# Kernel optimization log

Measured on AMD Instinct MI355X. Metric: run time of the kernel, lower is better.

Reference implementation:

```python
import jax, jax.numpy as jnp
import numpy as np

B, M, SV, OV, R, L, V, E = 256, 10, 32, 32, 128, 12, 1000, 64
M2 = M * M
STATE_DIM = (SV + 1) * M2  # 3300
OBJ_DIM = OV * M2          # 3200


def setup_inputs() -> dict:
    key = jax.random.key(0)
    ks = jax.random.split(key, 24)
    s = 0.02
    inp = {
        "state": jax.random.randint(ks[0], (B, M2), 0, SV),
        "obj": jax.random.randint(ks[1], (B, M2), 0, OV),
        "text": jax.random.randint(ks[2], (B, L), 0, V),
        # state MLP [STATE_DIM,128,128,R]
        "Ws1": jax.random.normal(ks[3], (STATE_DIM, 128)) * s,
        "bs1": jnp.zeros((128,)),
        "Ws2": jax.random.normal(ks[4], (128, 128)) * s,
        "bs2": jnp.zeros((128,)),
        "Ws3": jax.random.normal(ks[5], (128, R)) * s,
        "bs3": jnp.zeros((R,)),
        # object MLP [OBJ_DIM,128,128,R]
        "Wo1": jax.random.normal(ks[6], (OBJ_DIM, 128)) * s,
        "bo1": jnp.zeros((128,)),
        "Wo2": jax.random.normal(ks[7], (128, 128)) * s,
        "bo2": jnp.zeros((128,)),
        "Wo3": jax.random.normal(ks[8], (128, R)) * s,
        "bo3": jnp.zeros((R,)),
        # LSTM text encoder: embedding + single-layer LSTM with hidden=R
        "emb": jax.random.normal(ks[9], (V, E)) * s,
        "Wih": jax.random.normal(ks[10], (E, 4 * R)) * s,
        "Whh": jax.random.normal(ks[11], (R, 4 * R)) * s,
        "b_lstm": jnp.zeros((4 * R,)),
    }
    return inp


def _mlp(x, W1, b1, W2, b2, W3, b3):
    h = jax.nn.relu(x @ W1 + b1)
    h = jax.nn.relu(h @ W2 + b2)
    return h @ W3 + b3


def _lstm_last_hidden(text, emb, Wih, Whh, b):
    # text: (B, L) ids -> final hidden (B, R)
    x = emb[text]                      # (B, L, E)
    xs = jnp.swapaxes(x, 0, 1)         # (L, B, E)
    h0 = jnp.zeros((text.shape[0], R), x.dtype)
    c0 = jnp.zeros((text.shape[0], R), x.dtype)

    def step(carry, xt):
        h, c = carry
        g = xt @ Wih + h @ Whh + b     # (B, 4R)
        i, f, gg, o = jnp.split(g, 4, axis=-1)
        c = jax.nn.sigmoid(f) * c + jax.nn.sigmoid(i) * jnp.tanh(gg)
        h = jax.nn.sigmoid(o) * jnp.tanh(c)
        return (h, c), None

    (h, _), _ = jax.lax.scan(step, (h0, c0), xs)
    return h


def reference(state, obj, text, Ws1, bs1, Ws2, bs2, Ws3, bs3,
              Wo1, bo1, Wo2, bo2, Wo3, bo3, emb, Wih, Whh, b_lstm):
    b = state.shape[0]
    # one-hot encodings (torch scatter_ over channel dim)
    state_oh = jax.nn.one_hot(state, SV, dtype=jnp.float32)   # (B, 100, SV)
    obj_oh = jax.nn.one_hot(obj, OV, dtype=jnp.float32)       # (B, 100, OV)

    # repeat each map map_dim^2 times; copy p gets a one-hot of agent position p
    pos = jnp.eye(M2, dtype=jnp.float32)[None, :, :, None]    # (1, 100 copies, 100 cells, 1)
    state_rep = jnp.broadcast_to(state_oh[:, None], (b, M2, M2, SV))
    state_inp = jnp.concatenate(
        [state_rep, jnp.broadcast_to(pos, (b, M2, M2, 1))], axis=-1
    ).reshape(b * M2, STATE_DIM)
    obj_inp = jnp.broadcast_to(obj_oh[:, None], (b, M2, M2, OV)).reshape(b * M2, OBJ_DIM)

    state_out = _mlp(state_inp, Ws1, bs1, Ws2, bs2, Ws3, bs3)   # (B*100, R)
    object_out = _mlp(obj_inp, Wo1, bo1, Wo2, bo2, Wo3, bo3)    # (B*100, R)

    # text is identical across the 100 copies -> encode once, broadcast
    h = _lstm_last_hidden(text, emb, Wih, Whh, b_lstm)          # (B, R)
    lstm_out = jnp.broadcast_to(h[:, None], (b, M2, R)).reshape(b * M2, R)

    values = state_out * object_out * lstm_out                 # (B*100, R)
    map_pred = values.sum(1).reshape(b, M, M)
    return map_pred
```

## Files before the change

### kernel.cpp

```cpp
#include <hip/hip_runtime.h>


#define B_   256
#define M2_  100
#define R_   128
#define L_   12
#define E_   64

typedef _Float16 half2v __attribute__((ext_vector_type(2)));
typedef _Float16 f16x8  __attribute__((ext_vector_type(8)));
typedef float    f32x4  __attribute__((ext_vector_type(4)));

__device__ __forceinline__ float sigf(float x) { return 1.f / (1.f + expf(-x)); }

__device__ __forceinline__ uint pk16(float a, float b) {
    half2v h; h.x = (_Float16)a; h.y = (_Float16)b;
    return __builtin_bit_cast(uint, h);
}

#define PINU4(v) asm volatile("" : "+v"(v.x), "+v"(v.y), "+v"(v.z), "+v"(v.w));

__global__ __launch_bounds__(256) void pack_kernel(
    const float* __restrict__ Whh, const float* __restrict__ Wih,
    const float* __restrict__ Ws2, void* __restrict__ wsv)
{
    _Float16* WhhT = (_Float16*)wsv;
    _Float16* WihT = WhhT + 65536;
    uint*     W2P  = (uint*)(WihT + 32768);
    int g = blockIdx.x * 256 + threadIdx.x;
    if (g < 65536) {
        int r = g >> 9, c = g & 511;
        WhhT[c * 128 + r] = (_Float16)Whh[r * 512 + c];
    } else if (g < 65536 + 32768) {
        int g2 = g - 65536;
        int e = g2 >> 9, c = g2 & 511;
        WihT[c * 64 + e] = (_Float16)Wih[e * 512 + c];
    } else if (g < 65536 + 32768 + 8192) {
        int g3 = g - 65536 - 32768;
        int jp = g3 >> 7, kk = g3 & 127;
        W2P[g3] = pk16(Ws2[(2 * jp) * R_ + kk], Ws2[(2 * jp + 1) * R_ + kk]);
    }
}

__global__ __launch_bounds__(1024) __attribute__((amdgpu_waves_per_eu(4, 4)))
void k1_kernel(
    const int* __restrict__ state, const int* __restrict__ obj, const int* __restrict__ text,
    const float* __restrict__ Ws1, const float* __restrict__ bs1,
    const float* __restrict__ Wo1, const float* __restrict__ bo1,
    const float* __restrict__ Wo2, const float* __restrict__ bo2,
    const float* __restrict__ Wo3, const float* __restrict__ bo3,
    const float* __restrict__ emb, const float* __restrict__ b_lstm,
    const _Float16* __restrict__ WhhT, const _Float16* __restrict__ WihT,
    float* __restrict__ wsH, float* __restrict__ wsO3, float* __restrict__ wsBS)
{
    const int tid = threadIdx.x;
    __shared__ __align__(16) uint  U[9248];
    __shared__ __align__(16) float part[1024];
    __shared__ __align__(16) float hbuf[R_];
    __shared__ __align__(16) uint  hpair[R_ / 2];
    __shared__ __align__(16) float tmp[R_], tmp2[R_];
    __shared__ int idx[M2_], tids[L_];

    const int k = tid & 127, qq = tid >> 7;

    if (blockIdx.x < 256) {
        const int b    = blockIdx.x;
        const int lane = tid & 63;
        const int wv   = tid >> 6;
        const int m16  = lane & 15;
        const int kgrp = lane >> 4;
        float* xw   = (float*)U;
        float* xemb = (float*)(U + 8192);

        uint4 afu[2][4];
        #pragma unroll
        for (int tt = 0; tt < 2; ++tt) {
            int col = (2 * wv + tt) * 16 + m16;
            #pragma unroll
            for (int s = 0; s < 4; ++s) {
                afu[tt][s] = *(const uint4*)&WhhT[col * 128 + s * 32 + kgrp * 8];
                PINU4(afu[tt][s])
            }
        }

        if (tid < L_) tids[tid] = text[b * L_ + tid];
        if (tid >= 64 && tid < 128) hpair[tid - 64] = 0u;
        __syncthreads();
        if (tid < L_ * E_) xemb[(tid >> 6) * 66 + (tid & 63)] = emb[tids[tid >> 6] * E_ + (tid & 63)];
        else ((float*)(U + 8192 + 792))[tid - L_ * E_] = 0.f;
        __syncthreads();

        {
            f16x8 ax[2];
            #pragma unroll
            for (int s = 0; s < 2; ++s) {
                #pragma unroll
                for (int e = 0; e < 8; ++e)
                    ax[s][e] = (_Float16)xemb[m16 * 66 + s * 32 + kgrp * 8 + e];
            }
            #pragma unroll
            for (int h = 0; h < 2; ++h) {
                int col = (wv * 2 + h) * 16 + m16;
                float bl = b_lstm[col];
                f32x4 acc = { bl, bl, bl, bl };
                #pragma unroll
                for (int s = 0; s < 2; ++s) {
                    f16x8 bx = *(const f16x8*)&WihT[col * 64 + s * 32 + kgrp * 8];
                    acc = __builtin_amdgcn_mfma_f32_16x16x32_f16(ax[s], bx, acc, 0, 0, 0);
                }
                if (kgrp < 3) {
                    #pragma unroll
                    for (int r = 0; r < 4; ++r)
                        xw[(kgrp * 4 + r) * 512 + col] = acc[r];
                }
            }
        }
        __syncthreads();

        float cst = 0.f;
        for (int t = 0; t < L_; ++t) {
            f16x8 bf[4];
            #pragma unroll
            for (int s = 0; s < 4; ++s) {
                uint4 hb = *(const uint4*)&hpair[s * 16 + kgrp * 4];
                bf[s] = __builtin_bit_cast(f16x8, hb);
            }
            #pragma unroll
            for (int tt = 0; tt < 2; ++tt) {
                int colb = (2 * wv + tt) * 16 + kgrp * 4;
                f32x4 acc = *(const f32x4*)&xw[t * 512 + colb];
                #pragma unroll
                for (int s = 0; s < 4; ++s)
                    acc = __builtin_amdgcn_mfma_f32_16x16x32_f16(
                        __builtin_bit_cast(f16x8, afu[tt][s]), bf[s], acc, 0, 0, 0);
                if (m16 == 0) {
                    part[colb + 0] = acc[0];
                    part[colb + 1] = acc[1];
                    part[colb + 2] = acc[2];
                    part[colb + 3] = acc[3];
                }
            }
            __syncthreads();
            if (tid < R_) {
                float gi = part[tid], gf = part[R_ + tid], gg = part[2 * R_ + tid], go = part[3 * R_ + tid];
                cst = sigf(gf) * cst + sigf(gi) * tanhf(gg);
                float hn = sigf(go) * tanhf(cst);
                hbuf[tid] = hn;
                float hs = __shfl_down(hn, 1, 64);
                if (!(tid & 1)) hpair[tid >> 1] = pk16(hn, hs);
            }
            __syncthreads();
        }
        if (tid < R_) wsH[b * R_ + tid] = hbuf[tid];

    } else if (blockIdx.x < 512) {
        const int b = blockIdx.x - 256;
        if (tid < M2_) idx[tid] = obj[b * M2_ + tid];
        __syncthreads();
        {
            float acc = 0.f;
            int c0i = qq * 13, c1i = c0i + 13 < M2_ ? c0i + 13 : M2_;
            for (int c = c0i; c < c1i; ++c)
                acc += Wo1[(c * 32 + idx[c]) * R_ + k];
            part[qq * R_ + k] = acc;
        }
        __syncthreads();
        if (tid < R_) {
            float a = bo1[tid];
            #pragma unroll
            for (int q8 = 0; q8 < 8; ++q8) a += part[q8 * R_ + tid];
            tmp[tid] = fmaxf(a, 0.f);
        }
        __syncthreads();
        {
            float s0 = 0.f, s1 = 0.f, s2 = 0.f, s3 = 0.f;
            int j0 = qq * 16;
            #pragma unroll
            for (int j = 0; j < 16; j += 4) {
                s0 = fmaf(tmp[j0 + j + 0], Wo2[(j0 + j + 0) * R_ + k], s0);
                s1 = fmaf(tmp[j0 + j + 1], Wo2[(j0 + j + 1) * R_ + k], s1);
                s2 = fmaf(tmp[j0 + j + 2], Wo2[(j0 + j + 2) * R_ + k], s2);
                s3 = fmaf(tmp[j0 + j + 3], Wo2[(j0 + j + 3) * R_ + k], s3);
            }
            part[qq * R_ + k] = (s0 + s1) + (s2 + s3);
        }
        __syncthreads();
        if (tid < R_) {
            float a = bo2[tid];
            #pragma unroll
            for (int q8 = 0; q8 < 8; ++q8) a += part[q8 * R_ + tid];
            tmp2[tid] = fmaxf(a, 0.f);
        }
        __syncthreads();
        {
            float s0 = 0.f, s1 = 0.f, s2 = 0.f, s3 = 0.f;
            int j0 = qq * 16;
            #pragma unroll
            for (int j = 0; j < 16; j += 4) {
                s0 = fmaf(tmp2[j0 + j + 0], Wo3[(j0 + j + 0) * R_ + k], s0);
                s1 = fmaf(tmp2[j0 + j + 1], Wo3[(j0 + j + 1) * R_ + k], s1);
                s2 = fmaf(tmp2[j0 + j + 2], Wo3[(j0 + j + 2) * R_ + k], s2);
                s3 = fmaf(tmp2[j0 + j + 3], Wo3[(j0 + j + 3) * R_ + k], s3);
            }
            part[qq * R_ + k] = (s0 + s1) + (s2 + s3);
        }
        __syncthreads();
        if (tid < R_) {
            float a = bo3[tid];
            #pragma unroll
            for (int q8 = 0; q8 < 8; ++q8) a += part[q8 * R_ + tid];
            wsO3[b * R_ + tid] = a;
        }

    } else {
        const int b = blockIdx.x - 512;
        if (tid < M2_) idx[tid] = state[b * M2_ + tid];
        __syncthreads();
        {
            float acc = 0.f;
            int c0i = qq * 13, c1i = c0i + 13 < M2_ ? c0i + 13 : M2_;
            for (int c = c0i; c < c1i; ++c)
                acc += Ws1[(c * 33 + idx[c]) * R_ + k];
            part[qq * R_ + k] = acc;
        }
        __syncthreads();
        if (tid < R_) {
            float a = bs1[tid];
            #pragma unroll
            for (int q8 = 0; q8 < 8; ++q8) a += part[q8 * R_ + tid];
            wsBS[b * R_ + tid] = a;
        }
    }
}

__global__ __launch_bounds__(1024) __attribute__((amdgpu_waves_per_eu(4, 4)))
void k2_kernel(
    const float* __restrict__ Ws1, const float* __restrict__ bs2,
    const float* __restrict__ Ws3, const float* __restrict__ bs3,
    const uint* __restrict__ W2P,
    const float* __restrict__ wsH, const float* __restrict__ wsO3,
    const float* __restrict__ wsBS,
    float* __restrict__ out)
{
    const int b   = blockIdx.x;
    const int tid = threadIdx.x;

    __shared__ __align__(16) uint  U[16064];
    __shared__ __align__(16) float part[1024];
    __shared__ __align__(16) float wbuf[R_], ubuf[R_], bsbuf[R_];
    __shared__ float redw2[2][112];
    __shared__ float c0s;

    const int lane = tid & 63;
    const int wv   = tid >> 6;
    const int m16  = lane & 15;
    const int kgrp = lane >> 4;
    const int k = tid & 127, qq = tid >> 7;

    if (tid < R_) {
        wbuf[tid]  = wsH[b * R_ + tid] * wsO3[b * R_ + tid];
        bsbuf[tid] = wsBS[b * R_ + tid];
    }
    {
        const uint4* src = (const uint4*)W2P;
        #pragma unroll
        for (int idx = tid; idx < 2048; idx += 1024) {
            uint4 v = src[idx];
            int jp = idx >> 5, kq = idx & 31;
            *(uint4*)&U[jp * 132 + kq * 4] = v;
        }
    }
    __syncthreads();

    {
        float s0 = 0.f, s1 = 0.f, s2 = 0.f, s3 = 0.f;
        int j0 = qq * 16;
        const float4* w3 = reinterpret_cast<const float4*>(&Ws3[k * R_ + j0]);
        #pragma unroll
        for (int jj = 0; jj < 4; ++jj) {
            float4 v = w3[jj];
            s0 = fmaf(v.x, wbuf[j0 + jj * 4 + 0], s0);
            s1 = fmaf(v.y, wbuf[j0 + jj * 4 + 1], s1);
            s2 = fmaf(v.z, wbuf[j0 + jj * 4 + 2], s2);
            s3 = fmaf(v.w, wbuf[j0 + jj * 4 + 3], s3);
        }
        part[qq * R_ + k] = (s0 + s1) + (s2 + s3);
    }
    if (tid >= 960) {
        int j = tid - 960;
        float s = bs3[j] * wbuf[j] + bs3[j + 64] * wbuf[j + 64];
        s += __shfl_down(s, 32, 64);
        s += __shfl_down(s, 16, 64);
        s += __shfl_down(s, 8, 64);
        s += __shfl_down(s, 4, 64);
        s += __shfl_down(s, 2, 64);
        s += __shfl_down(s, 1, 64);
        if (j == 0) c0s = s;
    }
    #pragma unroll 4
    for (int pass = 0; pass < 13; ++pass) {
        int idx = pass * 1024 + tid;
        if (idx < M2_ * R_) {
            int j = idx & 127, p = idx >> 7;
            float v = fmaxf(bsbuf[j] + Ws1[(p * 33 + 32) * R_ + j], 0.f);
            float v2 = __shfl_down(v, 1, 64);
            if (!(j & 1)) U[8448 + p * 68 + (j >> 1)] = pk16(v, v2);
        }
    }
    if (tid < 816) U[8448 + 6800 + tid] = 0u;
    __syncthreads();
    if (tid < R_) {
        float a = 0.f;
        #pragma unroll
        for (int q8 = 0; q8 < 8; ++q8) a += part[q8 * R_ + tid];
        ubuf[tid] = a;
    }
    __syncthreads();

    if (wv < 14) {
        const int mtile = wv >> 1, nhalf = wv & 1;
        const uint* Ap = U + 8448 + (mtile * 16 + m16) * 68;
        f16x8 A[4];
        #pragma unroll
        for (int s = 0; s < 4; ++s)
            A[s] = __builtin_bit_cast(f16x8, *(const uint4*)&Ap[s * 16 + kgrp * 4]);
        f32x4 acc[4] = { {0,0,0,0}, {0,0,0,0}, {0,0,0,0}, {0,0,0,0} };
        #pragma unroll
        for (int nt = 0; nt < 4; ++nt) {
            int ko = (nhalf * 4 + nt) * 16 + m16;
            #pragma unroll
            for (int s = 0; s < 4; ++s) {
                const uint* Bp = U + (s * 16 + kgrp * 4) * 132 + ko;
                uint4 bv = { Bp[0], Bp[132], Bp[264], Bp[396] };
                acc[nt] = __builtin_amdgcn_mfma_f32_16x16x32_f16(
                    A[s], __builtin_bit_cast(f16x8, bv), acc[nt], 0, 0, 0);
            }
        }
        float vs0 = 0.f, vs1 = 0.f, vs2 = 0.f, vs3 = 0.f;
        #pragma unroll
        for (int nt = 0; nt < 4; ++nt) {
            int ko = (nhalf * 4 + nt) * 16 + m16;
            float bb = bs2[ko], uu = ubuf[ko];
            vs0 = fmaf(fmaxf(acc[nt][0] + bb, 0.f), uu, vs0);
            vs1 = fmaf(fmaxf(acc[nt][1] + bb, 0.f), uu, vs1);
            vs2 = fmaf(fmaxf(acc[nt][2] + bb, 0.f), uu, vs2);
            vs3 = fmaf(fmaxf(acc[nt][3] + bb, 0.f), uu, vs3);
        }
        vs0 += __shfl_xor(vs0, 1, 64); vs0 += __shfl_xor(vs0, 2, 64);
        vs0 += __shfl_xor(vs0, 4, 64); vs0 += __shfl_xor(vs0, 8, 64);
        vs1 += __shfl_xor(vs1, 1, 64); vs1 += __shfl_xor(vs1, 2, 64);
        vs1 += __shfl_xor(vs1, 4, 64); vs1 += __shfl_xor(vs1, 8, 64);
        vs2 += __shfl_xor(vs2, 1, 64); vs2 += __shfl_xor(vs2, 2, 64);
        vs2 += __shfl_xor(vs2, 4, 64); vs2 += __shfl_xor(vs2, 8, 64);
        vs3 += __shfl_xor(vs3, 1, 64); vs3 += __shfl_xor(vs3, 2, 64);
        vs3 += __shfl_xor(vs3, 4, 64); vs3 += __shfl_xor(vs3, 8, 64);
        if (m16 == 0) {
            int pr = mtile * 16 + kgrp * 4;
            redw2[nhalf][pr + 0] = vs0;
            redw2[nhalf][pr + 1] = vs1;
            redw2[nhalf][pr + 2] = vs2;
            redw2[nhalf][pr + 3] = vs3;
        }
    }
    __syncthreads();

    if (tid < M2_)
        out[b * M2_ + tid] = c0s + redw2[0][tid] + redw2[1][tid];
}

extern "C" void kernel_launch(void* const* d_in, const int* in_sizes, int n_in,
                              void* d_out, int out_size, void* d_ws, size_t ws_size,
                              hipStream_t stream) {
    const int*   state  = (const int*)d_in[0];
    const int*   obj    = (const int*)d_in[1];
    const int*   text   = (const int*)d_in[2];
    const float* Ws1    = (const float*)d_in[3];
    const float* bs1    = (const float*)d_in[4];
    const float* Ws2    = (const float*)d_in[5];
    const float* bs2    = (const float*)d_in[6];
    const float* Ws3    = (const float*)d_in[7];
    const float* bs3    = (const float*)d_in[8];
    const float* Wo1    = (const float*)d_in[9];
    const float* bo1    = (const float*)d_in[10];
    const float* Wo2    = (const float*)d_in[11];
    const float* bo2    = (const float*)d_in[12];
    const float* Wo3    = (const float*)d_in[13];
    const float* bo3    = (const float*)d_in[14];
    const float* emb    = (const float*)d_in[15];
    const float* Wih    = (const float*)d_in[16];
    const float* Whh    = (const float*)d_in[17];
    const float* b_lstm = (const float*)d_in[18];
    float* out = (float*)d_out;

    _Float16* WhhT = (_Float16*)d_ws;
    _Float16* WihT = WhhT + 65536;
    uint*     W2P  = (uint*)(WihT + 32768);
    float*    wsH  = (float*)(W2P + 8192);
    float*    wsO3 = wsH + 32768;
    float*    wsBS = wsO3 + 32768;

    hipLaunchKernelGGL(pack_kernel, dim3(416), dim3(256), 0, stream, Whh, Wih, Ws2, d_ws);
    hipLaunchKernelGGL(k1_kernel, dim3(768), dim3(1024), 0, stream,
                       state, obj, text, Ws1, bs1,
                       Wo1, bo1, Wo2, bo2, Wo3, bo3, emb, b_lstm,
                       WhhT, WihT, wsH, wsO3, wsBS);
    hipLaunchKernelGGL(k2_kernel, dim3(B_), dim3(1024), 0, stream,
                       Ws1, bs2, Ws3, bs3, W2P, wsH, wsO3, wsBS, out);
}
```

Baseline: 42.38 us.

## Halve block sizes, fuse LSTM gates in-register, move H1 build into k1

```diff
diff --git a/kernel.cpp b/kernel.cpp
--- a/kernel.cpp
+++ b/kernel.cpp
@@ -42,7 +42,7 @@
     }
 }
 
-__global__ __launch_bounds__(1024) __attribute__((amdgpu_waves_per_eu(4, 4)))
+__global__ __launch_bounds__(512) __attribute__((amdgpu_waves_per_eu(4, 4)))
 void k1_kernel(
     const int* __restrict__ state, const int* __restrict__ obj, const int* __restrict__ text,
     const float* __restrict__ Ws1, const float* __restrict__ bs1,
@@ -51,17 +51,14 @@
     const float* __restrict__ Wo3, const float* __restrict__ bo3,
     const float* __restrict__ emb, const float* __restrict__ b_lstm,
     const _Float16* __restrict__ WhhT, const _Float16* __restrict__ WihT,
-    float* __restrict__ wsH, float* __restrict__ wsO3, float* __restrict__ wsBS)
+    float* __restrict__ wsH, float* __restrict__ wsO3, uint* __restrict__ wsH1)
 {
     const int tid = threadIdx.x;
-    __shared__ __align__(16) uint  U[9248];
-    __shared__ __align__(16) float part[1024];
-    __shared__ __align__(16) float hbuf[R_];
-    __shared__ __align__(16) uint  hpair[R_ / 2];
-    __shared__ __align__(16) float tmp[R_], tmp2[R_];
+    __shared__ __align__(16) uint  U[7232];
+    __shared__ __align__(16) uint  hpair[2][64];
+    __shared__ __align__(16) float part[512];
+    __shared__ __align__(16) float tmp[R_], tmp2[R_], bsb[R_];
     __shared__ int idx[M2_], tids[L_];
-
-    const int k = tid & 127, qq = tid >> 7;
 
     if (blockIdx.x < 256) {
         const int b    = blockIdx.x;
@@ -70,37 +67,38 @@
         const int m16  = lane & 15;
         const int kgrp = lane >> 4;
         float* xw   = (float*)U;
-        float* xemb = (float*)(U + 8192);
-
-        uint4 afu[2][4];
-        #pragma unroll
-        for (int tt = 0; tt < 2; ++tt) {
-            int col = (2 * wv + tt) * 16 + m16;
+        float* xemb = (float*)(U + 6144);
+
+        uint4 afu[4][4];
+        #pragma unroll
+        for (int g = 0; g < 4; ++g) {
+            int col = (wv + 8 * g) * 16 + m16;
             #pragma unroll
             for (int s = 0; s < 4; ++s) {
-                afu[tt][s] = *(const uint4*)&WhhT[col * 128 + s * 32 + kgrp * 8];
-                PINU4(afu[tt][s])
+                afu[g][s] = *(const uint4*)&WhhT[col * 128 + s * 32 + kgrp * 8];
+                PINU4(afu[g][s])
             }
         }
 
         if (tid < L_) tids[tid] = text[b * L_ + tid];
-        if (tid >= 64 && tid < 128) hpair[tid - 64] = 0u;
-        __syncthreads();
-        if (tid < L_ * E_) xemb[(tid >> 6) * 66 + (tid & 63)] = emb[tids[tid >> 6] * E_ + (tid & 63)];
-        else ((float*)(U + 8192 + 792))[tid - L_ * E_] = 0.f;
+        if (tid >= 64 && tid < 128) hpair[0][tid - 64] = 0u;
+        __syncthreads();
+        for (int i = tid; i < 16 * 68; i += 512) {
+            int t = i / 68, c = i - t * 68;
+            xemb[i] = (c < 64 && t < L_) ? emb[tids[t] * E_ + c] : 0.f;
+        }
         __syncthreads();
 
         {
             f16x8 ax[2];
             #pragma unroll
-            for (int s = 0; s < 2; ++s) {
+            for (int s = 0; s < 2; ++s)
                 #pragma unroll
                 for (int e = 0; e < 8; ++e)
-                    ax[s][e] = (_Float16)xemb[m16 * 66 + s * 32 + kgrp * 8 + e];
-            }
-            #pragma unroll
-            for (int h = 0; h < 2; ++h) {
-                int col = (wv * 2 + h) * 16 + m16;
+                    ax[s][e] = (_Float16)xemb[m16 * 68 + s * 32 + kgrp * 8 + e];
+            #pragma unroll
+            for (int i4 = 0; i4 < 4; ++i4) {
+                int col = (wv + 8 * i4) * 16 + m16;
                 float bl = b_lstm[col];
                 f32x4 acc = { bl, bl, bl, bl };
                 #pragma unroll
@@ -117,66 +115,67 @@
         }
         __syncthreads();
 
-        float cst = 0.f;
+        float cst0 = 0.f, cst1 = 0.f, cst2 = 0.f, cst3 = 0.f;
+        float h0 = 0.f, h1v = 0.f, h2v = 0.f, h3v = 0.f;
         for (int t = 0; t < L_; ++t) {
+            const uint* hp = hpair[t & 1];
             f16x8 bf[4];
             #pragma unroll
-            for (int s = 0; s < 4; ++s) {
-                uint4 hb = *(const uint4*)&hpair[s * 16 + kgrp * 4];
-                bf[s] = __builtin_bit_cast(f16x8, hb);
-            }
-            #pragma unroll
-            for (int tt = 0; tt < 2; ++tt) {
-                int colb = (2 * wv + tt) * 16 + kgrp * 4;
-                f32x4 acc = *(const f32x4*)&xw[t * 512 + colb];
+            for (int s = 0; s < 4; ++s)
+                bf[s] = __builtin_bit_cast(f16x8, *(const uint4*)&hp[s * 16 + kgrp * 4]);
+            f32x4 acc[4];
+            #pragma unroll
+            for (int g = 0; g < 4; ++g) {
+                acc[g] = *(const f32x4*)&xw[t * 512 + (wv + 8 * g) * 16 + kgrp * 4];
                 #pragma unroll
                 for (int s = 0; s < 4; ++s)
-                    acc = __builtin_amdgcn_mfma_f32_16x16x32_f16(
-                        __builtin_bit_cast(f16x8, afu[tt][s]), bf[s], acc, 0, 0, 0);
-                if (m16 == 0) {
-                    part[colb + 0] = acc[0];
-                    part[colb + 1] = acc[1];
-                    part[colb + 2] = acc[2];
-                    part[colb + 3] = acc[3];
-                }
+                    acc[g] = __builtin_amdgcn_mfma_f32_16x16x32_f16(
+                        __builtin_bit_cast(f16x8, afu[g][s]), bf[s], acc[g], 0, 0, 0);
+            }
+            cst0 = sigf(acc[1][0]) * cst0 + sigf(acc[0][0]) * tanhf(acc[2][0]);
+            h0   = sigf(acc[3][0]) * tanhf(cst0);
+            cst1 = sigf(acc[1][1]) * cst1 + sigf(acc[0][1]) * tanhf(acc[2][1]);
+            h1v  = sigf(acc[3][1]) * tanhf(cst1);
+            cst2 = sigf(acc[1][2]) * cst2 + sigf(acc[0][2]) * tanhf(acc[2][2]);
+            h2v  = sigf(acc[3][2]) * tanhf(cst2);
+            cst3 = sigf(acc[1][3]) * cst3 + sigf(acc[0][3]) * tanhf(acc[2][3]);
+            h3v  = sigf(acc[3][3]) * tanhf(cst3);
+            if (m16 == 0) {
+                uint* hw = hpair[(t + 1) & 1];
+                hw[8 * wv + kgrp * 2]     = pk16(h0, h1v);
+                hw[8 * wv + kgrp * 2 + 1] = pk16(h2v, h3v);
             }
             __syncthreads();
-            if (tid < R_) {
-                float gi = part[tid], gf = part[R_ + tid], gg = part[2 * R_ + tid], go = part[3 * R_ + tid];
-                cst = sigf(gf) * cst + sigf(gi) * tanhf(gg);
-                float hn = sigf(go) * tanhf(cst);
-                hbuf[tid] = hn;
-                float hs = __shfl_down(hn, 1, 64);
-                if (!(tid & 1)) hpair[tid >> 1] = pk16(hn, hs);
-            }
-            __syncthreads();
-        }
-        if (tid < R_) wsH[b * R_ + tid] = hbuf[tid];
-
-    } else if (blockIdx.x < 512) {
+        }
+        if (m16 == 0) {
+            int j = wv * 16 + kgrp * 4;
+            wsH[b * R_ + j + 0] = h0;
+            wsH[b * R_ + j + 1] = h1v;
+            wsH[b * R_ + j + 2] = h2v;
+            wsH[b * R_ + j + 3] = h3v;
+        }
+
+    } else {
         const int b = blockIdx.x - 256;
+        const int k = tid & 127, qq = tid >> 7;
         if (tid < M2_) idx[tid] = obj[b * M2_ + tid];
         __syncthreads();
         {
-            float acc = 0.f;
-            int c0i = qq * 13, c1i = c0i + 13 < M2_ ? c0i + 13 : M2_;
-            for (int c = c0i; c < c1i; ++c)
-                acc += Wo1[(c * 32 + idx[c]) * R_ + k];
-            part[qq * R_ + k] = acc;
-        }
-        __syncthreads();
-        if (tid < R_) {
-            float a = bo1[tid];
-            #pragma unroll
-            for (int q8 = 0; q8 < 8; ++q8) a += part[q8 * R_ + tid];
-            tmp[tid] = fmaxf(a, 0.f);
-        }
+            float a = 0.f;
+            #pragma unroll 5
+            for (int c = qq * 25; c < qq * 25 + 25; ++c)
+                a += Wo1[(c * 32 + idx[c]) * R_ + k];
+            part[qq * R_ + k] = a;
+        }
+        __syncthreads();
+        if (tid < R_)
+            tmp[tid] = fmaxf(bo1[tid] + part[tid] + part[R_ + tid] + part[2 * R_ + tid] + part[3 * R_ + tid], 0.f);
         __syncthreads();
         {
             float s0 = 0.f, s1 = 0.f, s2 = 0.f, s3 = 0.f;
-            int j0 = qq * 16;
-            #pragma unroll
-            for (int j = 0; j < 16; j += 4) {
+            int j0 = qq * 32;
+            #pragma unroll
+            for (int j = 0; j < 32; j += 4) {
                 s0 = fmaf(tmp[j0 + j + 0], Wo2[(j0 + j + 0) * R_ + k], s0);
                 s1 = fmaf(tmp[j0 + j + 1], Wo2[(j0 + j + 1) * R_ + k], s1);
                 s2 = fmaf(tmp[j0 + j + 2], Wo2[(j0 + j + 2) * R_ + k], s2);
@@ -185,18 +184,14 @@
             part[qq * R_ + k] = (s0 + s1) + (s2 + s3);
         }
         __syncthreads();
-        if (tid < R_) {
-            float a = bo2[tid];
-            #pragma unroll
-            for (int q8 = 0; q8 < 8; ++q8) a += part[q8 * R_ + tid];
-            tmp2[tid] = fmaxf(a, 0.f);
-        }
+        if (tid < R_)
+            tmp2[tid] = fmaxf(bo2[tid] + part[tid] + part[R_ + tid] + part[2 * R_ + tid] + part[3 * R_ + tid], 0.f);
         __syncthreads();
         {
             float s0 = 0.f, s1 = 0.f, s2 = 0.f, s3 = 0.f;
-            int j0 = qq * 16;
-            #pragma unroll
-            for (int j = 0; j < 16; j += 4) {
+            int j0 = qq * 32;
+            #pragma unroll
+            for (int j = 0; j < 32; j += 4) {
                 s0 = fmaf(tmp2[j0 + j + 0], Wo3[(j0 + j + 0) * R_ + k], s0);
                 s1 = fmaf(tmp2[j0 + j + 1], Wo3[(j0 + j + 1) * R_ + k], s1);
                 s2 = fmaf(tmp2[j0 + j + 2], Wo3[(j0 + j + 2) * R_ + k], s2);
@@ -205,50 +200,48 @@
             part[qq * R_ + k] = (s0 + s1) + (s2 + s3);
         }
         __syncthreads();
-        if (tid < R_) {
-            float a = bo3[tid];
-            #pragma unroll
-            for (int q8 = 0; q8 < 8; ++q8) a += part[q8 * R_ + tid];
-            wsO3[b * R_ + tid] = a;
-        }
-
-    } else {
-        const int b = blockIdx.x - 512;
+        if (tid < R_)
+            wsO3[b * R_ + tid] = bo3[tid] + part[tid] + part[R_ + tid] + part[2 * R_ + tid] + part[3 * R_ + tid];
+        __syncthreads();
         if (tid < M2_) idx[tid] = state[b * M2_ + tid];
         __syncthreads();
         {
-            float acc = 0.f;
-            int c0i = qq * 13, c1i = c0i + 13 < M2_ ? c0i + 13 : M2_;
-            for (int c = c0i; c < c1i; ++c)
-                acc += Ws1[(c * 33 + idx[c]) * R_ + k];
-            part[qq * R_ + k] = acc;
-        }
-        __syncthreads();
-        if (tid < R_) {
-            float a = bs1[tid];
-            #pragma unroll
-            for (int q8 = 0; q8 < 8; ++q8) a += part[q8 * R_ + tid];
-            wsBS[b * R_ + tid] = a;
-        }
-    }
-}
-
-__global__ __launch_bounds__(1024) __attribute__((amdgpu_waves_per_eu(4, 4)))
+            float a = 0.f;
+            #pragma unroll 5
+            for (int c = qq * 25; c < qq * 25 + 25; ++c)
+                a += Ws1[(c * 33 + idx[c]) * R_ + k];
+            part[qq * R_ + k] = a;
+        }
+        __syncthreads();
+        if (tid < R_)
+            bsb[tid] = bs1[tid] + part[tid] + part[R_ + tid] + part[2 * R_ + tid] + part[3 * R_ + tid];
+        __syncthreads();
+        #pragma unroll 5
+        for (int pass = 0; pass < 25; ++pass) {
+            int id2 = pass * 512 + tid;
+            int j = id2 & 127, p = id2 >> 7;
+            float v = fmaxf(bsb[j] + Ws1[(p * 33 + 32) * R_ + j], 0.f);
+            float v2 = __shfl_down(v, 1, 64);
+            if (!(j & 1)) wsH1[(size_t)b * 7616 + p * 68 + (j >> 1)] = pk16(v, v2);
+        }
+    }
+}
+
+__global__ __launch_bounds__(512)
 void k2_kernel(
-    const float* __restrict__ Ws1, const float* __restrict__ bs2,
-    const float* __restrict__ Ws3, const float* __restrict__ bs3,
-    const uint* __restrict__ W2P,
+    const float* __restrict__ bs2, const float* __restrict__ Ws3,
+    const float* __restrict__ bs3, const uint* __restrict__ W2P,
     const float* __restrict__ wsH, const float* __restrict__ wsO3,
-    const float* __restrict__ wsBS,
+    const uint* __restrict__ wsH1,
     float* __restrict__ out)
 {
     const int b   = blockIdx.x;
     const int tid = threadIdx.x;
 
     __shared__ __align__(16) uint  U[16064];
-    __shared__ __align__(16) float part[1024];
-    __shared__ __align__(16) float wbuf[R_], ubuf[R_], bsbuf[R_];
-    __shared__ float redw2[2][112];
+    __shared__ __align__(16) float part[512];
+    __shared__ __align__(16) float wbuf[R_], ubuf[R_];
+    __shared__ float redw[112];
     __shared__ float c0s;
 
     const int lane = tid & 63;
@@ -257,37 +250,40 @@
     const int kgrp = lane >> 4;
     const int k = tid & 127, qq = tid >> 7;
 
-    if (tid < R_) {
-        wbuf[tid]  = wsH[b * R_ + tid] * wsO3[b * R_ + tid];
-        bsbuf[tid] = wsBS[b * R_ + tid];
-    }
+    if (tid < R_) wbuf[tid] = wsH[b * R_ + tid] * wsO3[b * R_ + tid];
     {
         const uint4* src = (const uint4*)W2P;
         #pragma unroll
-        for (int idx = tid; idx < 2048; idx += 1024) {
-            uint4 v = src[idx];
-            int jp = idx >> 5, kq = idx & 31;
+        for (int i = tid; i < 2048; i += 512) {
+            uint4 v = src[i];
+            int jp = i >> 5, kq = i & 31;
             *(uint4*)&U[jp * 132 + kq * 4] = v;
         }
+    }
+    {
+        const uint4* hsrc = (const uint4*)(wsH1 + (size_t)b * 7616);
+        uint4* hdst = (uint4*)(U + 8448);
+        #pragma unroll 4
+        for (int i = tid; i < 1700; i += 512) hdst[i] = hsrc[i];
     }
     __syncthreads();
 
     {
         float s0 = 0.f, s1 = 0.f, s2 = 0.f, s3 = 0.f;
-        int j0 = qq * 16;
-        const float4* w3 = reinterpret_cast<const float4*>(&Ws3[k * R_ + j0]);
-        #pragma unroll
-        for (int jj = 0; jj < 4; ++jj) {
-            float4 v = w3[jj];
-            s0 = fmaf(v.x, wbuf[j0 + jj * 4 + 0], s0);
-            s1 = fmaf(v.y, wbuf[j0 + jj * 4 + 1], s1);
-            s2 = fmaf(v.z, wbuf[j0 + jj * 4 + 2], s2);
-            s3 = fmaf(v.w, wbuf[j0 + jj * 4 + 3], s3);
+        const float4* w4 = reinterpret_cast<const float4*>(&Ws3[k * R_ + qq * 32]);
+        #pragma unroll
+        for (int jj = 0; jj < 8; ++jj) {
+            float4 v = w4[jj];
+            int j0 = qq * 32 + jj * 4;
+            s0 = fmaf(v.x, wbuf[j0 + 0], s0);
+            s1 = fmaf(v.y, wbuf[j0 + 1], s1);
+            s2 = fmaf(v.z, wbuf[j0 + 2], s2);
+            s3 = fmaf(v.w, wbuf[j0 + 3], s3);
         }
         part[qq * R_ + k] = (s0 + s1) + (s2 + s3);
     }
-    if (tid >= 960) {
-        int j = tid - 960;
+    if (tid >= 448) {
+        int j = tid - 448;
         float s = bs3[j] * wbuf[j] + bs3[j + 64] * wbuf[j + 64];
         s += __shfl_down(s, 32, 64);
         s += __shfl_down(s, 16, 64);
@@ -297,37 +293,23 @@
         s += __shfl_down(s, 1, 64);
         if (j == 0) c0s = s;
     }
-    #pragma unroll 4
-    for (int pass = 0; pass < 13; ++pass) {
-        int idx = pass * 1024 + tid;
-        if (idx < M2_ * R_) {
-            int j = idx & 127, p = idx >> 7;
-            float v = fmaxf(bsbuf[j] + Ws1[(p * 33 + 32) * R_ + j], 0.f);
-            float v2 = __shfl_down(v, 1, 64);
-            if (!(j & 1)) U[8448 + p * 68 + (j >> 1)] = pk16(v, v2);
-        }
-    }
-    if (tid < 816) U[8448 + 6800 + tid] = 0u;
     __syncthreads();
-    if (tid < R_) {
-        float a = 0.f;
-        #pragma unroll
-        for (int q8 = 0; q8 < 8; ++q8) a += part[q8 * R_ + tid];
-        ubuf[tid] = a;
-    }
+    if (tid < R_)
+        ubuf[tid] = part[tid] + part[R_ + tid] + part[2 * R_ + tid] + part[3 * R_ + tid];
     __syncthreads();
 
-    if (wv < 14) {
-        const int mtile = wv >> 1, nhalf = wv & 1;
-        const uint* Ap = U + 8448 + (mtile * 16 + m16) * 68;
+    if (wv < 7) {
+        const uint* Ap = U + 8448 + (wv * 16 + m16) * 68;
         f16x8 A[4];
         #pragma unroll
         for (int s = 0; s < 4; ++s)
             A[s] = __builtin_bit_cast(f16x8, *(const uint4*)&Ap[s * 16 + kgrp * 4]);
-        f32x4 acc[4] = { {0,0,0,0}, {0,0,0,0}, {0,0,0,0}, {0,0,0,0} };
-        #pragma unroll
-        for (int nt = 0; nt < 4; ++nt) {
-            int ko = (nhalf * 4 + nt) * 16 + m16;
+        f32x4 acc[8];
+        #pragma unroll
+        for (int nt = 0; nt < 8; ++nt) acc[nt] = f32x4{ 0.f, 0.f, 0.f, 0.f };
+        #pragma unroll
+        for (int nt = 0; nt < 8; ++nt) {
+            int ko = nt * 16 + m16;
             #pragma unroll
             for (int s = 0; s < 4; ++s) {
                 const uint* Bp = U + (s * 16 + kgrp * 4) * 132 + ko;
@@ -338,8 +320,8 @@
         }
         float vs0 = 0.f, vs1 = 0.f, vs2 = 0.f, vs3 = 0.f;
         #pragma unroll
-        for (int nt = 0; nt < 4; ++nt) {
-            int ko = (nhalf * 4 + nt) * 16 + m16;
+        for (int nt = 0; nt < 8; ++nt) {
+            int ko = nt * 16 + m16;
             float bb = bs2[ko], uu = ubuf[ko];
             vs0 = fmaf(fmaxf(acc[nt][0] + bb, 0.f), uu, vs0);
             vs1 = fmaf(fmaxf(acc[nt][1] + bb, 0.f), uu, vs1);
@@ -355,17 +337,17 @@
         vs3 += __shfl_xor(vs3, 1, 64); vs3 += __shfl_xor(vs3, 2, 64);
         vs3 += __shfl_xor(vs3, 4, 64); vs3 += __shfl_xor(vs3, 8, 64);
         if (m16 == 0) {
-            int pr = mtile * 16 + kgrp * 4;
-            redw2[nhalf][pr + 0] = vs0;
-            redw2[nhalf][pr + 1] = vs1;
-            redw2[nhalf][pr + 2] = vs2;
-            redw2[nhalf][pr + 3] = vs3;
+            int pr = wv * 16 + kgrp * 4;
+            redw[pr + 0] = vs0;
+            redw[pr + 1] = vs1;
+            redw[pr + 2] = vs2;
+            redw[pr + 3] = vs3;
         }
     }
     __syncthreads();
 
     if (tid < M2_)
-        out[b * M2_ + tid] = c0s + redw2[0][tid] + redw2[1][tid];
+        out[b * M2_ + tid] = c0s + redw[tid];
 }
 
 extern "C" void kernel_launch(void* const* d_in, const int* in_sizes, int n_in,
@@ -397,13 +379,13 @@
     uint*     W2P  = (uint*)(WihT + 32768);
     float*    wsH  = (float*)(W2P + 8192);
     float*    wsO3 = wsH + 32768;
-    float*    wsBS = wsO3 + 32768;
+    uint*     wsH1 = (uint*)(wsO3 + 32768);
 
     hipLaunchKernelGGL(pack_kernel, dim3(416), dim3(256), 0, stream, Whh, Wih, Ws2, d_ws);
-    hipLaunchKernelGGL(k1_kernel, dim3(768), dim3(1024), 0, stream,
+    hipLaunchKernelGGL(k1_kernel, dim3(512), dim3(512), 0, stream,
                        state, obj, text, Ws1, bs1,
                        Wo1, bo1, Wo2, bo2, Wo3, bo3, emb, b_lstm,
-                       WhhT, WihT, wsH, wsO3, wsBS);
-    hipLaunchKernelGGL(k2_kernel, dim3(B_), dim3(1024), 0, stream,
-                       Ws1, bs2, Ws3, bs3, W2P, wsH, wsO3, wsBS, out);
-}
+                       WhhT, WihT, wsH, wsO3, wsH1);
+    hipLaunchKernelGGL(k2_kernel, dim3(B_), dim3(512), 0, stream,
+                       bs2, Ws3, bs3, W2P, wsH, wsO3, wsH1, out);
+}
```

Result: slower. 47.09 us (+11.1%).
